# Kernel optimization log

Hardware: AMD Instinct MI355X
Metric: run time of the kernel (lower is better)

Reference implementation:

```python
import jax, jax.numpy as jnp
import numpy as np

H = 1024       # hidden_size
NH = 16        # num heads
HD = H // NH   # head dim
EPS = 1e-12


def setup_inputs() -> dict:
    key = jax.random.key(0)
    ks = jax.random.split(key, 12)
    s = 1.0 / np.sqrt(H)
    return {
        "hidden_states": jax.random.normal(ks[0], (2, 2048, H), jnp.float32),
        "attention_mask": jnp.zeros((2, 1, 1, 2048), jnp.float32),
        "wq": jax.random.uniform(ks[1], (H, H), jnp.float32, -s, s),
        "bq": jnp.zeros((H,), jnp.float32),
        "wk": jax.random.uniform(ks[2], (H, H), jnp.float32, -s, s),
        "bk": jnp.zeros((H,), jnp.float32),
        "wv": jax.random.uniform(ks[3], (H, H), jnp.float32, -s, s),
        "bv": jnp.zeros((H,), jnp.float32),
        "wo": jax.random.uniform(ks[4], (H, H), jnp.float32, -s, s),
        "bo": jnp.zeros((H,), jnp.float32),
        "ln_gamma": jnp.ones((H,), jnp.float32),
        "ln_beta": jnp.zeros((H,), jnp.float32),
    }


def reference(hidden_states, attention_mask, wq, bq, wk, bk, wv, bv, wo, bo, ln_gamma, ln_beta):
    residual = hidden_states
    # pre-LayerNorm
    mu = jnp.mean(hidden_states, axis=-1, keepdims=True)
    var = jnp.var(hidden_states, axis=-1, keepdims=True)
    x = (hidden_states - mu) / jnp.sqrt(var + EPS) * ln_gamma + ln_beta

    B, S, _ = x.shape
    # QKV projections (torch Linear: x @ W.T + b), split heads -> [B, NH, S, HD]
    def proj(w, b):
        return (x @ w.T + b).reshape(B, S, NH, HD).transpose(0, 2, 1, 3)
    q = proj(wq, bq)
    k = proj(wk, bk)
    v = proj(wv, bv)

    scores = jnp.einsum("bhqd,bhkd->bhqk", q, k) / np.sqrt(HD).astype(np.float32)
    scores = scores + attention_mask  # broadcast additive mask
    probs = jax.nn.softmax(scores, axis=-1)
    ctx = jnp.einsum("bhqk,bhkd->bhqd", probs, v)
    ctx = ctx.transpose(0, 2, 1, 3).reshape(B, S, NH * HD)

    out = ctx @ wo.T + bo
    return out + residual
```

## Files before the change

### kernel.cpp

```cpp
#include <hip/hip_runtime.h>
#include <cstdint>

typedef unsigned short u16;
typedef __bf16  bf16x8 __attribute__((ext_vector_type(8)));
typedef unsigned short u16x8 __attribute__((ext_vector_type(8)));
typedef unsigned short u16x4 __attribute__((ext_vector_type(4)));
typedef float   f32x4  __attribute__((ext_vector_type(4)));
typedef float   f32x16 __attribute__((ext_vector_type(16)));

#define LOG2E 1.44269504088896340736f

__device__ __forceinline__ u16 f2b(float f) {
  union { __bf16 h; u16 u; } c; c.h = (__bf16)f;
  return c.u;
}

__device__ __forceinline__ int swz(int row) { return (row & 7) ^ ((row >> 3) & 7); }
__device__ __forceinline__ int sidx(int row, int k) {
  return row * 64 + ((((k >> 3) ^ swz(row)) & 7) << 3) + (k & 7);
}
__device__ __forceinline__ bf16x8 ld_frag(const u16* base, int row, int k) {
  return *(const bf16x8*)(base + sidx(row, k));
}

__device__ __forceinline__ void async16(const u16* g, u16* l) {
  __builtin_amdgcn_global_load_lds(
      (__attribute__((address_space(1))) unsigned int*)(uintptr_t)g,
      (__attribute__((address_space(3))) unsigned int*)(uintptr_t)l,
      16, 0, 0);
}

__device__ __forceinline__ void plswap(unsigned int &a, unsigned int &b) {
  auto r = __builtin_amdgcn_permlane32_swap(a, b, false, false);
  a = r[0]; b = r[1];
}

__global__ __launch_bounds__(256) void prep_kernel(
    const float* __restrict__ hs, const float* __restrict__ gamma,
    const float* __restrict__ beta, u16* __restrict__ X,
    const float* __restrict__ w0, const float* __restrict__ w1,
    const float* __restrict__ w2, const float* __restrict__ w3,
    u16* __restrict__ Wd) {
  const int tid = threadIdx.x;
  if (blockIdx.x >= 4096) {
    const int idx4 = blockIdx.x - 4096;
    const int mat = idx4 >> 10;
    const float* src = (mat == 0) ? w0 : (mat == 1) ? w1 : (mat == 2) ? w2 : w3;
    const int idx = ((idx4 & 1023) * 256 + tid) * 4;
    f32x4 v = *(const f32x4*)(src + idx);
    u16x4 o;
#pragma unroll
    for (int j = 0; j < 4; ++j) o[j] = f2b(v[j]);
    *(u16x4*)(Wd + (size_t)mat * 1048576 + idx) = o;
    return;
  }
  __shared__ float red[8];
  const int row = blockIdx.x;
  f32x4 v = *(const f32x4*)(hs + (size_t)row * 1024 + tid * 4);
  float s = 0.f, s2 = 0.f;
#pragma unroll
  for (int j = 0; j < 4; ++j) { s += v[j]; s2 += v[j] * v[j]; }
#pragma unroll
  for (int o = 1; o < 64; o <<= 1) { s += __shfl_xor(s, o); s2 += __shfl_xor(s2, o); }
  const int wid = tid >> 6, lane = tid & 63;
  if (lane == 0) { red[wid] = s; red[4 + wid] = s2; }
  __syncthreads();
  s  = red[0] + red[1] + red[2] + red[3];
  s2 = red[4] + red[5] + red[6] + red[7];
  const float mean = s * (1.f / 1024.f);
  const float var  = fmaxf(s2 * (1.f / 1024.f) - mean * mean, 0.f);
  const float rstd = rsqrtf(var + 1e-12f);
  f32x4 g = *(const f32x4*)(gamma + tid * 4);
  f32x4 bb = *(const f32x4*)(beta + tid * 4);
  u16x4 outv;
#pragma unroll
  for (int j = 0; j < 4; ++j) outv[j] = f2b((v[j] - mean) * rstd * g[j] + bb[j]);
  *(u16x4*)(X + (size_t)row * 1024 + tid * 4) = outv;
}

template <int MODE>
__device__ __forceinline__ void gemm_tile_128(
    const u16* __restrict__ A, const u16* __restrict__ Bt,
    const float* __restrict__ bias, const float* __restrict__ res,
    void* __restrict__ Cv, int ldc, int m0, int nG) {
  __shared__ __align__(16) u16 As[128 * 64];
  __shared__ __align__(16) u16 Bs[128 * 64];
  const int tid = threadIdx.x;
  const int wid = tid >> 6;
  const int lane = tid & 63;
  const int l15 = lane & 15, lq = lane >> 4;
  const int wm = (wid & 1) << 6, wn = (wid >> 1) << 6;
  const int srow = tid >> 3;
  const int sg = tid & 7;

  f32x4 acc[4][4] = {};
  u16x8 ar[4], br[4];

#pragma unroll
  for (int i = 0; i < 4; ++i) {
    int row = (i << 5) + srow;
    ar[i] = *(const u16x8*)(A  + (size_t)row * 1024 + (sg << 3));
    br[i] = *(const u16x8*)(Bt + (size_t)row * 1024 + (sg << 3));
  }

  for (int k0 = 0; k0 < 1024; k0 += 64) {
    if (k0) __syncthreads();
#pragma unroll
    for (int i = 0; i < 4; ++i) {
      int row = (i << 5) + srow;
      *(u16x8*)(As + sidx(row, sg << 3)) = ar[i];
      *(u16x8*)(Bs + sidx(row, sg << 3)) = br[i];
    }
    __syncthreads();
    if (k0 + 64 < 1024) {
#pragma unroll
      for (int i = 0; i < 4; ++i) {
        int row = (i << 5) + srow;
        ar[i] = *(const u16x8*)(A  + (size_t)row * 1024 + k0 + 64 + (sg << 3));
        br[i] = *(const u16x8*)(Bt + (size_t)row * 1024 + k0 + 64 + (sg << 3));
      }
    }
#pragma unroll
    for (int kk = 0; kk < 2; ++kk) {
      bf16x8 af[4], bf[4];
#pragma unroll
      for (int mi = 0; mi < 4; ++mi) af[mi] = ld_frag(As, wm + (mi << 4) + l15, (kk << 5) + (lq << 3));
#pragma unroll
      for (int ni = 0; ni < 4; ++ni) bf[ni] = ld_frag(Bs, wn + (ni << 4) + l15, (kk << 5) + (lq << 3));
#pragma unroll
      for (int mi = 0; mi < 4; ++mi)
#pragma unroll
        for (int ni = 0; ni < 4; ++ni)
          acc[mi][ni] = __builtin_amdgcn_mfma_f32_16x16x32_bf16(af[mi], bf[ni], acc[mi][ni], 0, 0, 0);
    }
  }
  __syncthreads();

  if (MODE == 2) {
    u16* Rg = (wid < 2 ? As : Bs) + ((wid & 1) << 12);
#pragma unroll
    for (int ni = 0; ni < 4; ++ni) {
      const float bv = bias[wn + (ni << 4) + l15];
#pragma unroll
      for (int mi = 0; mi < 4; ++mi) {
        u16x4 pk;
#pragma unroll
        for (int r = 0; r < 4; ++r) pk[r] = f2b(acc[mi][ni][r] + bv);
        *(u16x4*)(Rg + sidx((ni << 4) + l15, (mi << 4) + (lq << 2))) = pk;
      }
    }
    __asm__ volatile("" ::: "memory");
    const int rrow = lane >> 3;
    const int rg8  = (lane & 7) << 3;
    const int mg0 = m0 + wm;
    const int bb = mg0 >> 11, ss0 = mg0 & 2047;
    const int hh = (nG + wn) >> 6;
    u16* vbase = (u16*)Cv + ((size_t)((bb << 4) + hh) * 64) * 2048 + ss0;
#pragma unroll
    for (int p = 0; p < 8; ++p) {
      const int nl = (p << 3) + rrow;
      bf16x8 rowv = ld_frag(Rg, nl, rg8);
      *(bf16x8*)(vbase + (size_t)nl * 2048 + rg8) = rowv;
    }
  } else {
#pragma unroll
    for (int ni = 0; ni < 4; ++ni) {
      const int n = wn + (ni << 4) + l15;
      const float bv = bias[n];
#pragma unroll
      for (int mi = 0; mi < 4; ++mi) {
#pragma unroll
        for (int r = 0; r < 4; ++r) {
          const int m = wm + (mi << 4) + (lq << 2) + r;
          float v = acc[mi][ni][r] + bv;
          if (MODE == 1) {
            v += res[(size_t)m * ldc + n];
            ((float*)Cv)[(size_t)m * ldc + n] = v;
          } else {
            ((u16*)Cv)[(size_t)m * ldc + n] = f2b(v);
          }
        }
      }
    }
  }
}

__global__ __launch_bounds__(256, 3) void qkv_kernel(
    const u16* __restrict__ X, const u16* __restrict__ W,
    const float* __restrict__ bq, const float* __restrict__ bk, const float* __restrict__ bv,
    u16* __restrict__ QK, u16* __restrict__ VT) {
  const int n0 = blockIdx.x << 7;
  const int m0 = blockIdx.y << 7;
  const int wsel = n0 >> 10;
  const int nloc = n0 & 1023;
  const u16* Bt = W + (size_t)wsel * 1048576 + (size_t)nloc * 1024;
  if (wsel < 2) {
    const float* bias = (wsel == 0 ? bq : bk) + nloc;
    gemm_tile_128<0>(X + (size_t)m0 * 1024, Bt, bias, nullptr,
                     QK + (size_t)m0 * 2048 + n0, 2048, 0, 0);
  } else {
    gemm_tile_128<2>(X + (size_t)m0 * 1024, Bt, bv + nloc, nullptr,
                     VT, 0, m0, nloc);
  }
}

__global__ __launch_bounds__(256, 3) void out_kernel(
    const u16* __restrict__ CTX, const u16* __restrict__ wo,
    const float* __restrict__ bo, const float* __restrict__ res, float* __restrict__ OUT) {
  const int n0 = blockIdx.x << 7;
  const int m0 = blockIdx.y << 7;
  gemm_tile_128<1>(CTX + (size_t)m0 * 1024, wo + (size_t)n0 * 1024, bo + n0,
                   res + (size_t)m0 * 1024 + n0, OUT + (size_t)m0 * 1024 + n0, 1024, 0, 0);
}

__global__ __launch_bounds__(256, 2) void attn_kernel(
    const u16* __restrict__ QK, const u16* __restrict__ VT,
    const float* __restrict__ mask, u16* __restrict__ CTX) {
  __shared__ __align__(16) u16 Ksb[2][64 * 64];
  __shared__ __align__(16) u16 Vtsb[2][64 * 64];
  const int tid = threadIdx.x;
  const int wid = tid >> 6;
  const int lane = tid & 63;
  const int l31 = lane & 31, b5 = lane >> 5;

  const int lid = blockIdx.x;
  const int sw = ((lid & 7) << 6) | (lid >> 3);
  const int qt = sw & 15;
  const int hz = sw >> 4;
  const int h = hz & 15;
  const int b = hz >> 4;

  const int qbase = (b << 11) + (qt << 7) + (wid << 5);
  const u16* Kbase  = QK + (size_t)(b << 11) * 2048 + 1024 + (h << 6);
  const u16* VTbase = VT + (size_t)(((b << 4) + h) << 6) * 2048;

  bf16x8 qf[4];
#pragma unroll
  for (int ds = 0; ds < 4; ++ds)
    qf[ds] = *(const bf16x8*)(QK + (size_t)(qbase + l31) * 2048 + (h << 6) + (ds << 4) + (b5 << 3));

  f32x16 cacc[2] = {};
  float l_run = 0.f;

  const int sg = lane & 7;
  const int srow0 = (wid << 4) + (lane >> 3);
  const int srow1 = srow0 + 8;
  const int gk0 = ((sg ^ swz(srow0)) & 7) << 3;
  const int gk1 = ((sg ^ swz(srow1)) & 7) << 3;
  const int ld0 = (wid << 10);
  const int ld1 = (wid << 10) + 512;

  async16(Kbase + (size_t)srow0 * 2048 + gk0, &Ksb[0][0] + ld0);
  async16(Kbase + (size_t)srow1 * 2048 + gk1, &Ksb[0][0] + ld1);
  async16(VTbase + (size_t)srow0 * 2048 + gk0, &Vtsb[0][0] + ld0);
  async16(VTbase + (size_t)srow1 * 2048 + gk1, &Vtsb[0][0] + ld1);

  const float c1 = 0.125f * LOG2E;

  for (int kt = 0; kt < 32; ++kt) {
    const u16* Ks  = &Ksb[kt & 1][0];
    const u16* Vts = &Vtsb[kt & 1][0];
    __syncthreads();
    if (kt + 1 < 32) {
      const int nk = (kt + 1) << 6;
      async16(Kbase + (size_t)(nk + srow0) * 2048 + gk0, &Ksb[(kt + 1) & 1][0] + ld0);
      async16(Kbase + (size_t)(nk + srow1) * 2048 + gk1, &Ksb[(kt + 1) & 1][0] + ld1);
      async16(VTbase + (size_t)srow0 * 2048 + nk + gk0, &Vtsb[(kt + 1) & 1][0] + ld0);
      async16(VTbase + (size_t)srow1 * 2048 + nk + gk1, &Vtsb[(kt + 1) & 1][0] + ld1);
    }

    f32x16 sacc[2] = {};
#pragma unroll
    for (int ds = 0; ds < 4; ++ds) {
      bf16x8 kf0 = ld_frag(Ks, l31,      (ds << 4) + (b5 << 3));
      bf16x8 kf1 = ld_frag(Ks, 32 + l31, (ds << 4) + (b5 << 3));
      sacc[0] = __builtin_amdgcn_mfma_f32_32x32x16_bf16(kf0, qf[ds], sacc[0], 0, 0, 0);
      sacc[1] = __builtin_amdgcn_mfma_f32_32x32x16_bf16(kf1, qf[ds], sacc[1], 0, 0, 0);
    }

    unsigned int pw[2][8];
#pragma unroll
    for (int ki = 0; ki < 2; ++ki) {
      float pv[16];
#pragma unroll
      for (int rr = 0; rr < 4; ++rr) {
        f32x4 mv = *(const f32x4*)(mask + (b << 11) + (kt << 6) + (ki << 5) + (rr << 3) + (b5 << 2));
#pragma unroll
        for (int c = 0; c < 4; ++c) {
          float p = __builtin_amdgcn_exp2f(sacc[ki][(rr << 2) + c] * c1 + mv[c] * LOG2E);
          pv[(rr << 2) + c] = p;
          l_run += p;
        }
      }
#pragma unroll
      for (int j = 0; j < 8; ++j) {
        unsigned int w;
        asm("v_cvt_pk_bf16_f32 %0, %1, %2" : "=v"(w) : "v"(pv[2 * j]), "v"(pv[2 * j + 1]));
        pw[ki][j] = w;
      }
      plswap(pw[ki][0], pw[ki][2]);
      plswap(pw[ki][1], pw[ki][3]);
      plswap(pw[ki][4], pw[ki][6]);
      plswap(pw[ki][5], pw[ki][7]);
    }

#pragma unroll
    for (int ki = 0; ki < 2; ++ki)
#pragma unroll
      for (int kb = 0; kb < 2; ++kb) {
        union { unsigned int u[4]; bf16x8 v; } pcvt;
#pragma unroll
        for (int j = 0; j < 4; ++j) pcvt.u[j] = pw[ki][(kb << 2) + j];
        const bf16x8 pf = pcvt.v;
#pragma unroll
        for (int dm = 0; dm < 2; ++dm) {
          bf16x8 vf = ld_frag(Vts, (dm << 5) + l31, (ki << 5) + (kb << 4) + (b5 << 3));
          cacc[dm] = __builtin_amdgcn_mfma_f32_32x32x16_bf16(vf, pf, cacc[dm], 0, 0, 0);
        }
      }
  }

  l_run += __shfl_xor(l_run, 32);
  const float inv = 1.0f / l_run;
  u16* Crow = CTX + (size_t)(qbase + l31) * 1024 + (h << 6);
#pragma unroll
  for (int dm = 0; dm < 2; ++dm)
#pragma unroll
    for (int rr = 0; rr < 4; ++rr) {
      u16x4 o;
#pragma unroll
      for (int c = 0; c < 4; ++c) o[c] = f2b(cacc[dm][(rr << 2) + c] * inv);
      *(u16x4*)(Crow + (dm << 5) + (rr << 3) + (b5 << 2)) = o;
    }
}

extern "C" void kernel_launch(void* const* d_in, const int* in_sizes, int n_in,
                              void* d_out, int out_size, void* d_ws, size_t ws_size,
                              hipStream_t stream) {
  const float* hs   = (const float*)d_in[0];
  const float* mask = (const float*)d_in[1];
  const float* wq   = (const float*)d_in[2];
  const float* bq   = (const float*)d_in[3];
  const float* wk   = (const float*)d_in[4];
  const float* bk   = (const float*)d_in[5];
  const float* wv   = (const float*)d_in[6];
  const float* bv   = (const float*)d_in[7];
  const float* wo   = (const float*)d_in[8];
  const float* bo   = (const float*)d_in[9];
  const float* lg   = (const float*)d_in[10];
  const float* lb   = (const float*)d_in[11];

  u16* X   = (u16*)d_ws;
  u16* QK  = X + (size_t)4096 * 1024;
  u16* CTX = QK + (size_t)4096 * 2048;
  u16* W   = CTX + (size_t)4096 * 1024;
  u16* VT  = W + (size_t)4 * 1048576;
  float* OUT = (float*)d_out;

  prep_kernel<<<8192, 256, 0, stream>>>(hs, lg, lb, X, wq, wk, wv, wo, W);
  qkv_kernel<<<dim3(24, 32), 256, 0, stream>>>(X, W, bq, bk, bv, QK, VT);
  attn_kernel<<<dim3(512), 256, 0, stream>>>(QK, VT, mask, CTX);
  out_kernel<<<dim3(8, 32), 256, 0, stream>>>(CTX, W + (size_t)3 * 1048576, bo, hs, OUT);
}
```

Before: 216.6 us.

## Split attention key range across two wave groups and combine via LDS

The attention block grows from 256 to 512 threads. Each half of the waves processes half of the key sequence, with its own double-buffered K/V tiles, and the partial context sums and row sums are merged through shared memory at the end. The P·V accumulation is also split into two independent accumulator chains so consecutive MFMAs do not depend on each other. The goal is more waves in flight per block and a shorter serial key loop, at the cost of doubled LDS, more registers, and an extra reduction step with two barriers.

```diff
diff --git a/kernel.cpp b/kernel.cpp
--- a/kernel.cpp
+++ b/kernel.cpp
@@ -213,13 +213,15 @@
                    res + (size_t)m0 * 1024 + n0, OUT + (size_t)m0 * 1024 + n0, 1024, 0, 0);
 }
 
-__global__ __launch_bounds__(256, 2) void attn_kernel(
+__global__ __launch_bounds__(512, 4) void attn_kernel(
     const u16* __restrict__ QK, const u16* __restrict__ VT,
     const float* __restrict__ mask, u16* __restrict__ CTX) {
-  __shared__ __align__(16) u16 Ksb[2][64 * 64];
-  __shared__ __align__(16) u16 Vtsb[2][64 * 64];
+  __shared__ __align__(16) u16 Ksb[2][2][64 * 64];
+  __shared__ __align__(16) u16 Vtsb[2][2][64 * 64];
   const int tid = threadIdx.x;
   const int wid = tid >> 6;
+  const int half = wid >> 2;
+  const int wid4 = wid & 3;
   const int lane = tid & 63;
   const int l31 = lane & 31, b5 = lane >> 5;
 
@@ -230,9 +232,10 @@
   const int h = hz & 15;
   const int b = hz >> 4;
 
-  const int qbase = (b << 11) + (qt << 7) + (wid << 5);
+  const int qbase = (b << 11) + (qt << 7) + (wid4 << 5);
   const u16* Kbase  = QK + (size_t)(b << 11) * 2048 + 1024 + (h << 6);
   const u16* VTbase = VT + (size_t)(((b << 4) + h) << 6) * 2048;
+  const int kh = half << 10;
 
   bf16x8 qf[4];
 #pragma unroll
@@ -240,33 +243,34 @@
     qf[ds] = *(const bf16x8*)(QK + (size_t)(qbase + l31) * 2048 + (h << 6) + (ds << 4) + (b5 << 3));
 
   f32x16 cacc[2] = {};
-  float l_run = 0.f;
+  f32x16 caccB[2] = {};
+  float l0 = 0.f, l1 = 0.f;
 
   const int sg = lane & 7;
-  const int srow0 = (wid << 4) + (lane >> 3);
+  const int srow0 = (wid4 << 4) + (lane >> 3);
   const int srow1 = srow0 + 8;
   const int gk0 = ((sg ^ swz(srow0)) & 7) << 3;
   const int gk1 = ((sg ^ swz(srow1)) & 7) << 3;
-  const int ld0 = (wid << 10);
-  const int ld1 = (wid << 10) + 512;
-
-  async16(Kbase + (size_t)srow0 * 2048 + gk0, &Ksb[0][0] + ld0);
-  async16(Kbase + (size_t)srow1 * 2048 + gk1, &Ksb[0][0] + ld1);
-  async16(VTbase + (size_t)srow0 * 2048 + gk0, &Vtsb[0][0] + ld0);
-  async16(VTbase + (size_t)srow1 * 2048 + gk1, &Vtsb[0][0] + ld1);
+  const int ld0 = (wid4 << 10);
+  const int ld1 = ld0 + 512;
+
+  async16(Kbase + (size_t)(kh + srow0) * 2048 + gk0, &Ksb[half][0][0] + ld0);
+  async16(Kbase + (size_t)(kh + srow1) * 2048 + gk1, &Ksb[half][0][0] + ld1);
+  async16(VTbase + (size_t)srow0 * 2048 + kh + gk0, &Vtsb[half][0][0] + ld0);
+  async16(VTbase + (size_t)srow1 * 2048 + kh + gk1, &Vtsb[half][0][0] + ld1);
 
   const float c1 = 0.125f * LOG2E;
 
-  for (int kt = 0; kt < 32; ++kt) {
-    const u16* Ks  = &Ksb[kt & 1][0];
-    const u16* Vts = &Vtsb[kt & 1][0];
+  for (int kt = 0; kt < 16; ++kt) {
+    const u16* Ks  = &Ksb[half][kt & 1][0];
+    const u16* Vts = &Vtsb[half][kt & 1][0];
     __syncthreads();
-    if (kt + 1 < 32) {
-      const int nk = (kt + 1) << 6;
-      async16(Kbase + (size_t)(nk + srow0) * 2048 + gk0, &Ksb[(kt + 1) & 1][0] + ld0);
-      async16(Kbase + (size_t)(nk + srow1) * 2048 + gk1, &Ksb[(kt + 1) & 1][0] + ld1);
-      async16(VTbase + (size_t)srow0 * 2048 + nk + gk0, &Vtsb[(kt + 1) & 1][0] + ld0);
-      async16(VTbase + (size_t)srow1 * 2048 + nk + gk1, &Vtsb[(kt + 1) & 1][0] + ld1);
+    if (kt + 1 < 16) {
+      const int nk = kh + ((kt + 1) << 6);
+      async16(Kbase + (size_t)(nk + srow0) * 2048 + gk0, &Ksb[half][(kt + 1) & 1][0] + ld0);
+      async16(Kbase + (size_t)(nk + srow1) * 2048 + gk1, &Ksb[half][(kt + 1) & 1][0] + ld1);
+      async16(VTbase + (size_t)srow0 * 2048 + nk + gk0, &Vtsb[half][(kt + 1) & 1][0] + ld0);
+      async16(VTbase + (size_t)srow1 * 2048 + nk + gk1, &Vtsb[half][(kt + 1) & 1][0] + ld1);
     }
 
     f32x16 sacc[2] = {};
@@ -282,16 +286,18 @@
 #pragma unroll
     for (int ki = 0; ki < 2; ++ki) {
       float pv[16];
+      float rs = 0.f;
 #pragma unroll
       for (int rr = 0; rr < 4; ++rr) {
-        f32x4 mv = *(const f32x4*)(mask + (b << 11) + (kt << 6) + (ki << 5) + (rr << 3) + (b5 << 2));
+        f32x4 mv = *(const f32x4*)(mask + (b << 11) + kh + (kt << 6) + (ki << 5) + (rr << 3) + (b5 << 2));
 #pragma unroll
         for (int c = 0; c < 4; ++c) {
           float p = __builtin_amdgcn_exp2f(sacc[ki][(rr << 2) + c] * c1 + mv[c] * LOG2E);
           pv[(rr << 2) + c] = p;
-          l_run += p;
+          rs += p;
         }
       }
+      if (ki == 0) l0 += rs; else l1 += rs;
 #pragma unroll
       for (int j = 0; j < 8; ++j) {
         unsigned int w;
@@ -315,23 +321,55 @@
 #pragma unroll
         for (int dm = 0; dm < 2; ++dm) {
           bf16x8 vf = ld_frag(Vts, (dm << 5) + l31, (ki << 5) + (kb << 4) + (b5 << 3));
-          cacc[dm] = __builtin_amdgcn_mfma_f32_32x32x16_bf16(vf, pf, cacc[dm], 0, 0, 0);
+          if (ki == 0)
+            cacc[dm]  = __builtin_amdgcn_mfma_f32_32x32x16_bf16(vf, pf, cacc[dm], 0, 0, 0);
+          else
+            caccB[dm] = __builtin_amdgcn_mfma_f32_32x32x16_bf16(vf, pf, caccB[dm], 0, 0, 0);
         }
       }
   }
 
-  l_run += __shfl_xor(l_run, 32);
-  const float inv = 1.0f / l_run;
-  u16* Crow = CTX + (size_t)(qbase + l31) * 1024 + (h << 6);
-#pragma unroll
-  for (int dm = 0; dm < 2; ++dm)
-#pragma unroll
-    for (int rr = 0; rr < 4; ++rr) {
-      u16x4 o;
-#pragma unroll
-      for (int c = 0; c < 4; ++c) o[c] = f2b(cacc[dm][(rr << 2) + c] * inv);
-      *(u16x4*)(Crow + (dm << 5) + (rr << 3) + (b5 << 2)) = o;
-    }
+  cacc[0] += caccB[0];
+  cacc[1] += caccB[1];
+  float l_run = l0 + l1;
+
+  float* CombC = (float*)&Ksb[0][0][0];
+  float* CombL = (float*)&Vtsb[0][0][0];
+  __syncthreads();
+  if (half == 1) {
+    float* dst = CombC + (wid4 << 11) + (lane << 5);
+#pragma unroll
+    for (int j = 0; j < 8; ++j) {
+      f32x4 t;
+#pragma unroll
+      for (int c = 0; c < 4; ++c) t[c] = cacc[j >> 2][((j & 3) << 2) + c];
+      *(f32x4*)(dst + (((j ^ swz(lane)) & 7) << 2)) = t;
+    }
+    CombL[(wid4 << 6) + lane] = l_run;
+  }
+  __syncthreads();
+  if (half == 0) {
+    float* src = CombC + (wid4 << 11) + (lane << 5);
+#pragma unroll
+    for (int j = 0; j < 8; ++j) {
+      f32x4 t = *(const f32x4*)(src + (((j ^ swz(lane)) & 7) << 2));
+#pragma unroll
+      for (int c = 0; c < 4; ++c) cacc[j >> 2][((j & 3) << 2) + c] += t[c];
+    }
+    l_run += CombL[(wid4 << 6) + lane];
+    l_run += __shfl_xor(l_run, 32);
+    const float inv = 1.0f / l_run;
+    u16* Crow = CTX + (size_t)(qbase + l31) * 1024 + (h << 6);
+#pragma unroll
+    for (int dm = 0; dm < 2; ++dm)
+#pragma unroll
+      for (int rr = 0; rr < 4; ++rr) {
+        u16x4 o;
+#pragma unroll
+        for (int c = 0; c < 4; ++c) o[c] = f2b(cacc[dm][(rr << 2) + c] * inv);
+        *(u16x4*)(Crow + (dm << 5) + (rr << 3) + (b5 << 2)) = o;
+      }
+  }
 }
 
 extern "C" void kernel_launch(void* const* d_in, const int* in_sizes, int n_in,
@@ -359,6 +397,6 @@
 
   prep_kernel<<<8192, 256, 0, stream>>>(hs, lg, lb, X, wq, wk, wv, wo, W);
   qkv_kernel<<<dim3(24, 32), 256, 0, stream>>>(X, W, bq, bk, bv, QK, VT);
-  attn_kernel<<<dim3(512), 256, 0, stream>>>(QK, VT, mask, CTX);
+  attn_kernel<<<dim3(512), 512, 0, stream>>>(QK, VT, mask, CTX);
   out_kernel<<<dim3(8, 32), 256, 0, stream>>>(CTX, W + (size_t)3 * 1048576, bo, hs, OUT);
 }
```

New measurement: 358.8 us. 1.66x slower.
